# Optimization experiments

Measured on AMD Instinct MI355X. Metric: run time of the kernel, lower is better.

The kernel has to match this reference:

```python
import jax, jax.numpy as jnp
import numpy as np


def setup_inputs() -> dict:
    key = jax.random.key(0)
    ks = jax.random.split(key, 6)
    T, B, N = 2048, 32, 1024
    return {
        "decoder_hx": jax.random.normal(ks[0], (B, N), dtype=jnp.float32),
        "encoder_outputs": jax.random.normal(ks[1], (T, B, N), dtype=jnp.float32),
        "encoder_feature": jax.random.normal(ks[2], (T, B, N), dtype=jnp.float32),
        "mask_tensor": jnp.ones((B, T), dtype=jnp.float32),
        "Ws_w": jax.random.normal(ks[3], (N, N), dtype=jnp.float32) / np.sqrt(N),
        "Ws_b": jnp.zeros((N,), dtype=jnp.float32),
        "v_w": jax.random.normal(ks[4], (1, N), dtype=jnp.float32) / np.sqrt(N),
        "v_b": jnp.zeros((1,), dtype=jnp.float32),
        "lin_w": jax.random.normal(ks[5], (N, 2 * N), dtype=jnp.float32) / np.sqrt(2 * N),
        "lin_b": jnp.zeros((N,), dtype=jnp.float32),
    }


def reference(decoder_hx, encoder_outputs, encoder_feature, mask_tensor,
              Ws_w, Ws_b, v_w, v_b, lin_w, lin_b):
    # Bahdanau additive attention.
    # dec_feature = W_s(decoder_hx): (b, n), broadcast over time t_k
    dec_feature = decoder_hx @ Ws_w.T + Ws_b                     # (b, n)
    e = jnp.tanh(encoder_feature + dec_feature[None, :, :])      # (t, b, n)
    # scores = v(e): rank-1 projection to a scalar per (t, b)
    scores = jnp.einsum('tbn,n->bt', e, v_w[0]) + v_b[0]         # (b, t)
    attn_dist = jax.nn.softmax(scores, axis=1) * mask_tensor     # (b, t)
    # weighted temporal sum of encoder outputs -> context vector
    content_vector = jnp.einsum('bt,tbn->bn', attn_dist, encoder_outputs)
    concat = jnp.concatenate([content_vector, decoder_hx], axis=1)  # (b, 2n)
    hx_attention = jnp.tanh(concat @ lin_w.T + lin_b)            # (b, n)
    return hx_attention
```

## Files before the change

### kernel.cpp

```cpp
#include <hip/hip_runtime.h>
#include <math.h>

#define T 2048
#define B 32
#define N 1024
#define NCHUNK 64
#define TCHUNK (T / NCHUNK)

__device__ __forceinline__ float fast_tanh(float x) {
    float e = __expf(2.0f * x);
    return 1.0f - 2.0f * __builtin_amdgcn_rcpf(e + 1.0f);
}

__device__ __forceinline__ float wave_reduce_sum(float v) {
    #pragma unroll
    for (int off = 32; off > 0; off >>= 1) v += __shfl_down(v, off, 64);
    return v;
}

__global__ void dec_feature_kernel(const float* __restrict__ hx,
                                   const float* __restrict__ Ws_w,
                                   const float* __restrict__ Ws_b,
                                   float* __restrict__ dec) {
    int w = blockIdx.x * 4 + (threadIdx.x >> 6);
    int lane = threadIdx.x & 63;
    int i = w >> 5;
    int b = w & 31;
    const float4* wr = (const float4*)(Ws_w + (size_t)i * N);
    const float4* hr = (const float4*)(hx + (size_t)b * N);
    float acc = 0.f;
    #pragma unroll
    for (int k = 0; k < 4; ++k) {
        float4 a = wr[k * 64 + lane];
        float4 h = hr[k * 64 + lane];
        acc += a.x * h.x + a.y * h.y + a.z * h.z + a.w * h.w;
    }
    acc = wave_reduce_sum(acc);
    if (lane == 0) dec[(size_t)b * N + i] = acc + Ws_b[i];
}

__global__ void scores_kernel(const float* __restrict__ ef,
                              const float* __restrict__ dec,
                              const float* __restrict__ v_w,
                              const float* __restrict__ v_b,
                              float* __restrict__ scores) {
    int w = blockIdx.x * 4 + (threadIdx.x >> 6);
    int lane = threadIdx.x & 63;
    int t = w >> 5;
    int b = w & 31;
    const float4* e4 = (const float4*)(ef + (size_t)w * N);
    const float4* d4 = (const float4*)(dec + (size_t)b * N);
    const float4* v4 = (const float4*)v_w;
    float acc = 0.f;
    #pragma unroll
    for (int k = 0; k < 4; ++k) {
        float4 e = e4[k * 64 + lane];
        float4 d = d4[k * 64 + lane];
        float4 v = v4[k * 64 + lane];
        acc += fast_tanh(e.x + d.x) * v.x + fast_tanh(e.y + d.y) * v.y
             + fast_tanh(e.z + d.z) * v.z + fast_tanh(e.w + d.w) * v.w;
    }
    acc = wave_reduce_sum(acc);
    if (lane == 0) scores[(size_t)b * T + t] = acc + v_b[0];
}

__global__ void softmax_kernel(const float* __restrict__ scores,
                               const float* __restrict__ mask,
                               float* __restrict__ attn) {
    int b = blockIdx.x;
    int tid = threadIdx.x;
    int lane = tid & 63, wid = tid >> 6;
    float s[8];
    float m = -1e30f;
    #pragma unroll
    for (int k = 0; k < 8; ++k) {
        s[k] = scores[(size_t)b * T + tid + k * 256];
        m = fmaxf(m, s[k]);
    }
    __shared__ float redm[4], reds[4];
    #pragma unroll
    for (int off = 32; off > 0; off >>= 1) m = fmaxf(m, __shfl_down(m, off, 64));
    if (lane == 0) redm[wid] = m;
    __syncthreads();
    m = fmaxf(fmaxf(redm[0], redm[1]), fmaxf(redm[2], redm[3]));
    float sum = 0.f;
    #pragma unroll
    for (int k = 0; k < 8; ++k) { s[k] = __expf(s[k] - m); sum += s[k]; }
    sum = wave_reduce_sum(sum);
    if (lane == 0) reds[wid] = sum;
    __syncthreads();
    float inv = __builtin_amdgcn_rcpf(reds[0] + reds[1] + reds[2] + reds[3]);
    #pragma unroll
    for (int k = 0; k < 8; ++k)
        attn[(size_t)b * T + tid + k * 256] =
            s[k] * inv * mask[(size_t)b * T + tid + k * 256];
}

__global__ void content_partial_kernel(const float* __restrict__ eo,
                                       const float* __restrict__ attn,
                                       float* __restrict__ partial) {
    int b = blockIdx.y;
    int chunk = blockIdx.x;
    int tid = threadIdx.x;
    const float4* base = (const float4*)eo;
    float4 acc = {0.f, 0.f, 0.f, 0.f};
    #pragma unroll 4
    for (int tt = 0; tt < TCHUNK; ++tt) {
        int t = chunk * TCHUNK + tt;
        float a = attn[(size_t)b * T + t];
        float4 e = base[((size_t)t * B + b) * (N / 4) + tid];
        acc.x += a * e.x; acc.y += a * e.y; acc.z += a * e.z; acc.w += a * e.w;
    }
    ((float4*)partial)[((size_t)chunk * B + b) * (N / 4) + tid] = acc;
}

__global__ void content_reduce_kernel(const float* __restrict__ partial,
                                      float* __restrict__ content) {
    int g = blockIdx.x * 256 + threadIdx.x;
    const float4* p4 = (const float4*)partial;
    float4 acc = {0.f, 0.f, 0.f, 0.f};
    #pragma unroll 8
    for (int c = 0; c < NCHUNK; ++c) {
        float4 v = p4[(size_t)c * (B * N / 4) + g];
        acc.x += v.x; acc.y += v.y; acc.z += v.z; acc.w += v.w;
    }
    ((float4*)content)[g] = acc;
}

__global__ void out_kernel(const float* __restrict__ content,
                           const float* __restrict__ hx,
                           const float* __restrict__ lin_w,
                           const float* __restrict__ lin_b,
                           float* __restrict__ out) {
    int w = blockIdx.x * 4 + (threadIdx.x >> 6);
    int lane = threadIdx.x & 63;
    int i = w >> 5;
    int b = w & 31;
    const float4* wr = (const float4*)(lin_w + (size_t)i * 2 * N);
    const float4* cr = (const float4*)(content + (size_t)b * N);
    const float4* hr = (const float4*)(hx + (size_t)b * N);
    float acc = 0.f;
    #pragma unroll
    for (int k = 0; k < 4; ++k) {
        float4 a = wr[k * 64 + lane];
        float4 c = cr[k * 64 + lane];
        acc += a.x * c.x + a.y * c.y + a.z * c.z + a.w * c.w;
    }
    #pragma unroll
    for (int k = 0; k < 4; ++k) {
        float4 a = wr[256 + k * 64 + lane];
        float4 h = hr[k * 64 + lane];
        acc += a.x * h.x + a.y * h.y + a.z * h.z + a.w * h.w;
    }
    acc = wave_reduce_sum(acc);
    if (lane == 0) out[(size_t)b * N + i] = fast_tanh(acc + lin_b[i]);
}

extern "C" void kernel_launch(void* const* d_in, const int* in_sizes, int n_in,
                              void* d_out, int out_size, void* d_ws, size_t ws_size,
                              hipStream_t stream) {
    const float* hx    = (const float*)d_in[0];
    const float* eo    = (const float*)d_in[1];
    const float* ef    = (const float*)d_in[2];
    const float* mask  = (const float*)d_in[3];
    const float* Ws_w  = (const float*)d_in[4];
    const float* Ws_b  = (const float*)d_in[5];
    const float* v_w   = (const float*)d_in[6];
    const float* v_b   = (const float*)d_in[7];
    const float* lin_w = (const float*)d_in[8];
    const float* lin_b = (const float*)d_in[9];
    float* out = (float*)d_out;

    float* ws      = (float*)d_ws;
    float* dec     = ws;
    float* scores  = dec + B * N;
    float* attn    = scores + B * T;
    float* content = attn + B * T;
    float* partial = content + B * N;

    dec_feature_kernel<<<(B * N) / 4, 256, 0, stream>>>(hx, Ws_w, Ws_b, dec);
    scores_kernel<<<(T * B) / 4, 256, 0, stream>>>(ef, dec, v_w, v_b, scores);
    softmax_kernel<<<B, 256, 0, stream>>>(scores, mask, attn);
    content_partial_kernel<<<dim3(NCHUNK, B), 256, 0, stream>>>(eo, attn, partial);
    content_reduce_kernel<<<(B * N / 4) / 256, 256, 0, stream>>>(partial, content);
    out_kernel<<<(B * N) / 4, 256, 0, stream>>>(content, hx, lin_w, lin_b, out);
}
```

Measured before the change: 562.0 us.

## Give each scores wave two rows, remap matvec indices, unroll content loop further

The scores kernel now has each wave process two (t,b) rows, one from each half of the time range, so the grid is halved and each wave has two independent loads in flight. The dec_feature and out matvec kernels reorder the wave-to-(i,b) mapping so that adjacent waves share the same batch vector and walk consecutive weight rows. The content partial loop unroll goes from 4 to 8. The aim is more memory-level parallelism in the bandwidth-bound scores pass, at the cost of higher register use per wave.

```diff
diff --git a/kernel.cpp b/kernel.cpp
--- a/kernel.cpp
+++ b/kernel.cpp
@@ -22,10 +22,10 @@
                                    const float* __restrict__ Ws_w,
                                    const float* __restrict__ Ws_b,
                                    float* __restrict__ dec) {
-    int w = blockIdx.x * 4 + (threadIdx.x >> 6);
+    int idx = blockIdx.x * 4 + (threadIdx.x >> 6);
     int lane = threadIdx.x & 63;
-    int i = w >> 5;
-    int b = w & 31;
+    int i = idx & (N - 1);
+    int b = idx >> 10;
     const float4* wr = (const float4*)(Ws_w + (size_t)i * N);
     const float4* hr = (const float4*)(hx + (size_t)b * N);
     float acc = 0.f;
@@ -48,20 +48,29 @@
     int lane = threadIdx.x & 63;
     int t = w >> 5;
     int b = w & 31;
-    const float4* e4 = (const float4*)(ef + (size_t)w * N);
+    const float4* e0 = (const float4*)(ef + (size_t)w * N);
+    const float4* e1 = (const float4*)(ef + ((size_t)w + T * B / 2) * N);
     const float4* d4 = (const float4*)(dec + (size_t)b * N);
     const float4* v4 = (const float4*)v_w;
-    float acc = 0.f;
+    float acc0 = 0.f, acc1 = 0.f;
     #pragma unroll
     for (int k = 0; k < 4; ++k) {
-        float4 e = e4[k * 64 + lane];
-        float4 d = d4[k * 64 + lane];
-        float4 v = v4[k * 64 + lane];
-        acc += fast_tanh(e.x + d.x) * v.x + fast_tanh(e.y + d.y) * v.y
-             + fast_tanh(e.z + d.z) * v.z + fast_tanh(e.w + d.w) * v.w;
+        float4 ea = e0[k * 64 + lane];
+        float4 eb = e1[k * 64 + lane];
+        float4 d  = d4[k * 64 + lane];
+        float4 v  = v4[k * 64 + lane];
+        acc0 += fast_tanh(ea.x + d.x) * v.x + fast_tanh(ea.y + d.y) * v.y
+              + fast_tanh(ea.z + d.z) * v.z + fast_tanh(ea.w + d.w) * v.w;
+        acc1 += fast_tanh(eb.x + d.x) * v.x + fast_tanh(eb.y + d.y) * v.y
+              + fast_tanh(eb.z + d.z) * v.z + fast_tanh(eb.w + d.w) * v.w;
     }
-    acc = wave_reduce_sum(acc);
-    if (lane == 0) scores[(size_t)b * T + t] = acc + v_b[0];
+    acc0 = wave_reduce_sum(acc0);
+    acc1 = wave_reduce_sum(acc1);
+    if (lane == 0) {
+        float vb = v_b[0];
+        scores[(size_t)b * T + t] = acc0 + vb;
+        scores[(size_t)b * T + t + T / 2] = acc1 + vb;
+    }
 }
 
 __global__ void softmax_kernel(const float* __restrict__ scores,
@@ -104,7 +113,7 @@
     int tid = threadIdx.x;
     const float4* base = (const float4*)eo;
     float4 acc = {0.f, 0.f, 0.f, 0.f};
-    #pragma unroll 4
+    #pragma unroll 8
     for (int tt = 0; tt < TCHUNK; ++tt) {
         int t = chunk * TCHUNK + tt;
         float a = attn[(size_t)b * T + t];
@@ -132,10 +141,10 @@
                            const float* __restrict__ lin_w,
                            const float* __restrict__ lin_b,
                            float* __restrict__ out) {
-    int w = blockIdx.x * 4 + (threadIdx.x >> 6);
+    int idx = blockIdx.x * 4 + (threadIdx.x >> 6);
     int lane = threadIdx.x & 63;
-    int i = w >> 5;
-    int b = w & 31;
+    int i = idx & (N - 1);
+    int b = idx >> 10;
     const float4* wr = (const float4*)(lin_w + (size_t)i * 2 * N);
     const float4* cr = (const float4*)(content + (size_t)b * N);
     const float4* hr = (const float4*)(hx + (size_t)b * N);
@@ -179,7 +188,7 @@
     float* partial = content + B * N;
 
     dec_feature_kernel<<<(B * N) / 4, 256, 0, stream>>>(hx, Ws_w, Ws_b, dec);
-    scores_kernel<<<(T * B) / 4, 256, 0, stream>>>(ef, dec, v_w, v_b, scores);
+    scores_kernel<<<(T * B / 2) / 4, 256, 0, stream>>>(ef, dec, v_w, v_b, scores);
     softmax_kernel<<<B, 256, 0, stream>>>(scores, mask, attn);
     content_partial_kernel<<<dim3(NCHUNK, B), 256, 0, stream>>>(eo, attn, partial);
     content_reduce_kernel<<<(B * N / 4) / 256, 256, 0, stream>>>(partial, content);
```

Measured after the change: 563.5 us. No clear change (+0.3%).
